# Kernel tuning notes

Measured on AMD Instinct MI355X. Metric: run time of the kernel, lower is better.

## Reference

```python
import jax, jax.numpy as jnp
import numpy as np

BATCH, G, E, D = 8192, 3, 32, 128  # batch, genres-per-sample, num experts, feature dim


def setup_inputs() -> dict:
    key = jax.random.key(0)
    k1, k2, k3, k4 = jax.random.split(key, 4)
    x = jax.random.normal(k1, (BATCH, D), dtype=jnp.float32)
    genres = jax.random.randint(k2, (BATCH, G), 0, E, dtype=jnp.int64)
    W0 = jax.random.normal(k3, (E, D, D), dtype=jnp.float32)
    W1 = jax.random.normal(k4, (E, D, D), dtype=jnp.float32)
    return {"x": x, "genres": genres, "W0": W0, "W1": W1}


def _moe_layer(x, genres, W):
    # gather per-token expert weights: [B, G, in, out]
    ew = W[genres]
    # mask: genre index 0 means padding slot
    mask = (genres != 0)[..., None].astype(x.dtype)  # [B, G, 1]
    # 'bij,bijk->bik' with x broadcast over the genre axis
    y = jnp.einsum('bi,bgio->bgo', x, ew) * mask      # [B, G, out]
    cnt = jnp.clip(jnp.sum(mask, axis=1), 1e-9)       # [B, 1]
    return jax.nn.leaky_relu(jnp.sum(y, axis=1) / cnt, negative_slope=0.01)


def reference(x, genres, W0, W1):
    x = _moe_layer(x, genres, W0)
    x = _moe_layer(x, genres, W1)
    return x
```

## Files before the change

kernel.cpp:

```cpp
#include <hip/hip_runtime.h>

#define BATCH 8192
#define NG 3
#define NE 32
#define D 128
#define NPAIR (BATCH * NG)
#define TILE 32
#define CHUNK 2048
#define NCHUNK (NPAIR / CHUNK)
#define NFIN (BATCH * 16 / 256)

typedef __attribute__((ext_vector_type(8))) short short8;
typedef __attribute__((ext_vector_type(4))) float f32x4;

#define OFF_YB   0
#define OFF_YB2  ((size_t)NPAIR * D * 2)
#define WS_REQUIRED (OFF_YB2 + (size_t)NPAIR * D * 2)

static __device__ __forceinline__ ushort f2bf(float f) {
    unsigned b = __float_as_uint(f);
    unsigned r = (b + 0x7FFFu + ((b >> 16) & 1u)) >> 16;
    return (ushort)r;
}
static __device__ __forceinline__ float bf2f(ushort u) {
    return __uint_as_float(((unsigned)u) << 16);
}
static __device__ __forceinline__ unsigned pk2(float lo, float hi) {
    return (unsigned)f2bf(lo) | ((unsigned)f2bf(hi) << 16);
}

template<int LAYER>
static __device__ __forceinline__ void gemm_body(
    const float* __restrict__ x, const ushort* __restrict__ ybin,
    const int* __restrict__ genres, const float* __restrict__ W,
    ushort* __restrict__ ydst)
{
    const int e = blockIdx.y + 1;
    const int pbase = blockIdx.x * CHUNK;

    __shared__ ushort sW[D * D];
    __shared__ ushort sX[TILE * D];
    __shared__ int list[CHUNK];
    __shared__ int scnt;

    const int tid = threadIdx.x;
    if (tid == 0) scnt = 0;
    __syncthreads();

    #pragma unroll
    for (int i = 0; i < CHUNK / 256; ++i) {
        int p = pbase + i * 256 + tid;
        if (genres[p] == e) {
            int idx = atomicAdd(&scnt, 1);
            list[idx] = p;
        }
    }

    const float* Ws = W + (size_t)e * D * D;
    char* sWb = (char*)sW;
    #pragma unroll
    for (int i = 0; i < 16; ++i) {
        int idx = i * 256 + tid;
        int c = idx & 127;
        int k4 = idx >> 7;
        float a0 = Ws[(size_t)(4 * k4 + 0) * D + c];
        float a1 = Ws[(size_t)(4 * k4 + 1) * D + c];
        float a2 = Ws[(size_t)(4 * k4 + 2) * D + c];
        float a3 = Ws[(size_t)(4 * k4 + 3) * D + c];
        int byteoff = (c * 256 + k4 * 8) ^ ((c & 7) << 4);
        uint2 q = { pk2(a0, a1), pk2(a2, a3) };
        *(uint2*)(sWb + byteoff) = q;
    }
    __syncthreads();

    const int ntotal = scnt;
    const int wave = tid >> 6, lane = tid & 63;
    const int g = lane >> 4, l15 = lane & 15;
    char* sXb = (char*)sX;

    for (int t0 = 0; t0 < ntotal; t0 += TILE) {
        const int nt = min(TILE, ntotal - t0);
        __syncthreads();

        {
            const int t = tid >> 3, th = tid & 7;
            int p = list[t0 + ((t < nt) ? t : 0)];
            int row = p / NG;
            int g0 = genres[row * NG + 0];
            int g1 = genres[row * NG + 1];
            int g2 = genres[row * NG + 2];
            int cnt = (g0 != 0) + (g1 != 0) + (g2 != 0);
            float scale = 1.0f / (float)((cnt > 0) ? cnt : 1);
            unsigned q[8];
            if (LAYER == 1) {
                const float* xp = x + (size_t)row * D + th * 16;
                float v[16];
                *(float4*)&v[0]  = *(const float4*)(xp);
                *(float4*)&v[4]  = *(const float4*)(xp + 4);
                *(float4*)&v[8]  = *(const float4*)(xp + 8);
                *(float4*)&v[12] = *(const float4*)(xp + 12);
                #pragma unroll
                for (int j = 0; j < 8; ++j)
                    q[j] = pk2(v[2*j] * scale, v[2*j+1] * scale);
            } else {
                float s[16];
                #pragma unroll
                for (int j = 0; j < 16; ++j) s[j] = 0.0f;
                #pragma unroll
                for (int slot = 0; slot < NG; ++slot) {
                    int gg = (slot == 0) ? g0 : (slot == 1) ? g1 : g2;
                    if (gg != 0) {
                        const ushort* yp = ybin + ((size_t)row * NG + slot) * D + th * 16;
                        uint4 va = *(const uint4*)yp;
                        uint4 vb = *(const uint4*)(yp + 8);
                        unsigned w[8] = { va.x, va.y, va.z, va.w,
                                          vb.x, vb.y, vb.z, vb.w };
                        #pragma unroll
                        for (int j = 0; j < 8; ++j) {
                            s[2*j]   += bf2f((ushort)(w[j] & 0xFFFF));
                            s[2*j+1] += bf2f((ushort)(w[j] >> 16));
                        }
                    }
                }
                #pragma unroll
                for (int j = 0; j < 8; ++j) {
                    float lo = s[2*j],  hi = s[2*j+1];
                    lo = ((lo >= 0.f) ? lo : 0.01f * lo) * scale;
                    hi = ((hi >= 0.f) ? hi : 0.01f * hi) * scale;
                    q[j] = pk2(lo, hi);
                }
            }
            int b0 = (t * 256 + (th * 2) * 16)     ^ ((t & 7) << 4);
            int b1 = (t * 256 + (th * 2 + 1) * 16) ^ ((t & 7) << 4);
            *(uint4*)(sXb + b0) = make_uint4(q[0], q[1], q[2], q[3]);
            *(uint4*)(sXb + b1) = make_uint4(q[4], q[5], q[6], q[7]);
        }
        __syncthreads();

        f32x4 acc00 = {0.f,0.f,0.f,0.f}, acc01 = {0.f,0.f,0.f,0.f};
        f32x4 acc10 = {0.f,0.f,0.f,0.f}, acc11 = {0.f,0.f,0.f,0.f};

        #pragma unroll
        for (int ks = 0; ks < 4; ++ks) {
            const int kb = ks * 64 + g * 16;
            int c0 = wave * 32 + l15, c1 = c0 + 16;
            short8 a0 = *(const short8*)(sWb + ((c0 * 256 + kb) ^ ((c0 & 7) << 4)));
            short8 a1 = *(const short8*)(sWb + ((c1 * 256 + kb) ^ ((c1 & 7) << 4)));
            int t0l = l15, t1l = l15 + 16;
            short8 b0 = *(const short8*)(sXb + ((t0l * 256 + kb) ^ ((t0l & 7) << 4)));
            short8 b1 = *(const short8*)(sXb + ((t1l * 256 + kb) ^ ((t1l & 7) << 4)));
            acc00 = __builtin_amdgcn_mfma_f32_16x16x32_bf16(a0, b0, acc00, 0, 0, 0);
            acc01 = __builtin_amdgcn_mfma_f32_16x16x32_bf16(a0, b1, acc01, 0, 0, 0);
            acc10 = __builtin_amdgcn_mfma_f32_16x16x32_bf16(a1, b0, acc10, 0, 0, 0);
            acc11 = __builtin_amdgcn_mfma_f32_16x16x32_bf16(a1, b1, acc11, 0, 0, 0);
        }

        #pragma unroll
        for (int n = 0; n < 2; ++n) {
            int tok = n * 16 + l15;
            if (tok < nt) {
                int p = list[t0 + tok];
                ushort* dst = ydst + (size_t)p * D + wave * 32 + g * 4;
                f32x4 v0 = (n == 0) ? acc00 : acc01;
                f32x4 v1 = (n == 0) ? acc10 : acc11;
                ushort4 p0 = { f2bf(v0[0]), f2bf(v0[1]), f2bf(v0[2]), f2bf(v0[3]) };
                ushort4 p1 = { f2bf(v1[0]), f2bf(v1[1]), f2bf(v1[2]), f2bf(v1[3]) };
                *(ushort4*)(dst)      = p0;
                *(ushort4*)(dst + 16) = p1;
            }
        }
    }
}

__global__ __launch_bounds__(256, 3) void moe_gemm1_kernel(
    const float* __restrict__ x, const int* __restrict__ genres,
    const float* __restrict__ W0, ushort* __restrict__ yb)
{
    gemm_body<1>(x, nullptr, genres, W0, yb);
}

__global__ __launch_bounds__(256, 3) void moe_gemm2_kernel(
    const ushort* __restrict__ yb, const int* __restrict__ genres,
    const float* __restrict__ W1, ushort* __restrict__ yb2)
{
    gemm_body<2>(nullptr, yb, genres, W1, yb2);
}

__global__ __launch_bounds__(256) void moe_final_kernel(
    const ushort* __restrict__ yb2, const int* __restrict__ genres,
    float* __restrict__ out)
{
    int gid = blockIdx.x * 256 + threadIdx.x;
    int b = gid >> 4, c8 = (gid & 15) * 8;
    int g0 = genres[b * NG + 0];
    int g1 = genres[b * NG + 1];
    int g2 = genres[b * NG + 2];

    float s[8] = {0,0,0,0,0,0,0,0};
    #pragma unroll
    for (int slot = 0; slot < NG; ++slot) {
        int g = (slot == 0) ? g0 : (slot == 1) ? g1 : g2;
        if (g != 0) {
            uint4 v = *(const uint4*)&yb2[((size_t)b * NG + slot) * D + c8];
            const unsigned w[4] = { v.x, v.y, v.z, v.w };
            #pragma unroll
            for (int j = 0; j < 4; ++j) {
                s[2*j]   += bf2f((ushort)(w[j] & 0xFFFF));
                s[2*j+1] += bf2f((ushort)(w[j] >> 16));
            }
        }
    }
    float r[8];
    #pragma unroll
    for (int j = 0; j < 8; ++j)
        r[j] = (s[j] >= 0.f) ? s[j] : 0.01f * s[j];
    float4 lo = { r[0], r[1], r[2], r[3] };
    float4 hi = { r[4], r[5], r[6], r[7] };
    *(float4*)&out[(size_t)b * D + c8]     = lo;
    *(float4*)&out[(size_t)b * D + c8 + 4] = hi;
}

__global__ __launch_bounds__(128) void moe_layer_kernel(
    const float* __restrict__ x, const int* __restrict__ genres,
    const float* __restrict__ W, float* __restrict__ out)
{
    const int b = blockIdx.x;
    const int o = threadIdx.x;
    __shared__ float xs[D];
    xs[o] = x[(size_t)b * D + o];
    __syncthreads();
    int e0 = genres[b * NG + 0], e1 = genres[b * NG + 1], e2 = genres[b * NG + 2];
    float acc = 0.0f; int cnt = 0;
    #pragma unroll
    for (int g = 0; g < NG; ++g) {
        int e = (g == 0) ? e0 : (g == 1) ? e1 : e2;
        if (e != 0) {
            ++cnt;
            const float* We = W + (size_t)e * D * D + o;
            float a = 0.0f;
            #pragma unroll 8
            for (int i = 0; i < D; ++i) a = fmaf(xs[i], We[(size_t)i * D], a);
            acc += a;
        }
    }
    float r = (cnt > 0) ? (acc / (float)cnt) : 0.0f;
    out[(size_t)b * D + o] = (r >= 0.0f) ? r : 0.01f * r;
}

extern "C" void kernel_launch(void* const* d_in, const int* in_sizes, int n_in,
                              void* d_out, int out_size, void* d_ws, size_t ws_size,
                              hipStream_t stream)
{
    const float* x      = (const float*)d_in[0];
    const int*   genres = (const int*)d_in[1];
    const float* W0     = (const float*)d_in[2];
    const float* W1     = (const float*)d_in[3];
    float*       out    = (float*)d_out;

    if (ws_size < WS_REQUIRED) {
        moe_layer_kernel<<<BATCH, D, 0, stream>>>(x,   genres, W0, out);
        moe_layer_kernel<<<BATCH, D, 0, stream>>>(out, genres, W1, out);
        return;
    }

    char* ws = (char*)d_ws;
    ushort* yb  = (ushort*)(ws + OFF_YB);
    ushort* yb2 = (ushort*)(ws + OFF_YB2);

    dim3 ggrid(NCHUNK, NE - 1);
    moe_gemm1_kernel<<<ggrid, 256, 0, stream>>>(x, genres, W0, yb);
    moe_gemm2_kernel<<<ggrid, 256, 0, stream>>>(yb, genres, W1, yb2);
    moe_final_kernel<<<NFIN, 256, 0, stream>>>(yb2, genres, out);
}
```

Measured before the change: 33.48 us.

## Split expert GEMM output columns across two blocks and vectorize genre scan

Each chunk/expert block now computes only half of the output columns, so the grid doubles and per-block shared weight storage halves, allowing higher occupancy (launch bounds raised to 4). The genre scan reads int4 vectors, and blocks with no matching tokens exit before loading weights. The cost is that the activation tile (gather, scale, leaky_relu for layer 2) is recomputed by both column halves, and each wave now issues fewer MFMAs per tile.

```diff
diff --git a/kernel.cpp b/kernel.cpp
--- a/kernel.cpp
+++ b/kernel.cpp
@@ -35,10 +35,12 @@
     const int* __restrict__ genres, const float* __restrict__ W,
     ushort* __restrict__ ydst)
 {
+    const int bx = blockIdx.x;
+    const int chunk = bx >> 1, hcol = bx & 1;
     const int e = blockIdx.y + 1;
-    const int pbase = blockIdx.x * CHUNK;
-
-    __shared__ ushort sW[D * D];
+    const int pbase = chunk * CHUNK;
+
+    __shared__ ushort sW[64 * D];
     __shared__ ushort sX[TILE * D];
     __shared__ int list[CHUNK];
     __shared__ int scnt;
@@ -47,22 +49,27 @@
     if (tid == 0) scnt = 0;
     __syncthreads();
 
-    #pragma unroll
-    for (int i = 0; i < CHUNK / 256; ++i) {
-        int p = pbase + i * 256 + tid;
-        if (genres[p] == e) {
-            int idx = atomicAdd(&scnt, 1);
-            list[idx] = p;
-        }
-    }
-
-    const float* Ws = W + (size_t)e * D * D;
+    const int4* g4 = (const int4*)(genres + pbase);
+    #pragma unroll
+    for (int i = 0; i < CHUNK / 1024; ++i) {
+        int4 gv = g4[i * 256 + tid];
+        int p = pbase + (i * 256 + tid) * 4;
+        if (gv.x == e) list[atomicAdd(&scnt, 1)] = p + 0;
+        if (gv.y == e) list[atomicAdd(&scnt, 1)] = p + 1;
+        if (gv.z == e) list[atomicAdd(&scnt, 1)] = p + 2;
+        if (gv.w == e) list[atomicAdd(&scnt, 1)] = p + 3;
+    }
+    __syncthreads();
+    const int ntotal = scnt;
+    if (ntotal == 0) return;
+
+    const float* Ws = W + (size_t)e * D * D + hcol * 64;
     char* sWb = (char*)sW;
     #pragma unroll
-    for (int i = 0; i < 16; ++i) {
+    for (int i = 0; i < 8; ++i) {
         int idx = i * 256 + tid;
-        int c = idx & 127;
-        int k4 = idx >> 7;
+        int c = idx & 63;
+        int k4 = idx >> 6;
         float a0 = Ws[(size_t)(4 * k4 + 0) * D + c];
         float a1 = Ws[(size_t)(4 * k4 + 1) * D + c];
         float a2 = Ws[(size_t)(4 * k4 + 2) * D + c];
@@ -71,11 +78,10 @@
         uint2 q = { pk2(a0, a1), pk2(a2, a3) };
         *(uint2*)(sWb + byteoff) = q;
     }
-    __syncthreads();
-
-    const int ntotal = scnt;
+
     const int wave = tid >> 6, lane = tid & 63;
     const int g = lane >> 4, l15 = lane & 15;
+    const int colb = wave * 16;
     char* sXb = (char*)sX;
 
     for (int t0 = 0; t0 < ntotal; t0 += TILE) {
@@ -137,22 +143,18 @@
         }
         __syncthreads();
 
-        f32x4 acc00 = {0.f,0.f,0.f,0.f}, acc01 = {0.f,0.f,0.f,0.f};
-        f32x4 acc10 = {0.f,0.f,0.f,0.f}, acc11 = {0.f,0.f,0.f,0.f};
+        f32x4 acc0 = {0.f,0.f,0.f,0.f}, acc1 = {0.f,0.f,0.f,0.f};
 
         #pragma unroll
         for (int ks = 0; ks < 4; ++ks) {
             const int kb = ks * 64 + g * 16;
-            int c0 = wave * 32 + l15, c1 = c0 + 16;
+            int c0 = colb + l15;
             short8 a0 = *(const short8*)(sWb + ((c0 * 256 + kb) ^ ((c0 & 7) << 4)));
-            short8 a1 = *(const short8*)(sWb + ((c1 * 256 + kb) ^ ((c1 & 7) << 4)));
             int t0l = l15, t1l = l15 + 16;
             short8 b0 = *(const short8*)(sXb + ((t0l * 256 + kb) ^ ((t0l & 7) << 4)));
             short8 b1 = *(const short8*)(sXb + ((t1l * 256 + kb) ^ ((t1l & 7) << 4)));
-            acc00 = __builtin_amdgcn_mfma_f32_16x16x32_bf16(a0, b0, acc00, 0, 0, 0);
-            acc01 = __builtin_amdgcn_mfma_f32_16x16x32_bf16(a0, b1, acc01, 0, 0, 0);
-            acc10 = __builtin_amdgcn_mfma_f32_16x16x32_bf16(a1, b0, acc10, 0, 0, 0);
-            acc11 = __builtin_amdgcn_mfma_f32_16x16x32_bf16(a1, b1, acc11, 0, 0, 0);
+            acc0 = __builtin_amdgcn_mfma_f32_16x16x32_bf16(a0, b0, acc0, 0, 0, 0);
+            acc1 = __builtin_amdgcn_mfma_f32_16x16x32_bf16(a0, b1, acc1, 0, 0, 0);
         }
 
         #pragma unroll
@@ -160,26 +162,23 @@
             int tok = n * 16 + l15;
             if (tok < nt) {
                 int p = list[t0 + tok];
-                ushort* dst = ydst + (size_t)p * D + wave * 32 + g * 4;
-                f32x4 v0 = (n == 0) ? acc00 : acc01;
-                f32x4 v1 = (n == 0) ? acc10 : acc11;
-                ushort4 p0 = { f2bf(v0[0]), f2bf(v0[1]), f2bf(v0[2]), f2bf(v0[3]) };
-                ushort4 p1 = { f2bf(v1[0]), f2bf(v1[1]), f2bf(v1[2]), f2bf(v1[3]) };
-                *(ushort4*)(dst)      = p0;
-                *(ushort4*)(dst + 16) = p1;
+                ushort* dst = ydst + (size_t)p * D + hcol * 64 + colb + g * 4;
+                f32x4 v = (n == 0) ? acc0 : acc1;
+                ushort4 pq = { f2bf(v[0]), f2bf(v[1]), f2bf(v[2]), f2bf(v[3]) };
+                *(ushort4*)dst = pq;
             }
         }
     }
 }
 
-__global__ __launch_bounds__(256, 3) void moe_gemm1_kernel(
+__global__ __launch_bounds__(256, 4) void moe_gemm1_kernel(
     const float* __restrict__ x, const int* __restrict__ genres,
     const float* __restrict__ W0, ushort* __restrict__ yb)
 {
     gemm_body<1>(x, nullptr, genres, W0, yb);
 }
 
-__global__ __launch_bounds__(256, 3) void moe_gemm2_kernel(
+__global__ __launch_bounds__(256, 4) void moe_gemm2_kernel(
     const ushort* __restrict__ yb, const int* __restrict__ genres,
     const float* __restrict__ W1, ushort* __restrict__ yb2)
 {
@@ -267,7 +266,7 @@
     ushort* yb  = (ushort*)(ws + OFF_YB);
     ushort* yb2 = (ushort*)(ws + OFF_YB2);
 
-    dim3 ggrid(NCHUNK, NE - 1);
+    dim3 ggrid(NCHUNK * 2, NE - 1);
     moe_gemm1_kernel<<<ggrid, 256, 0, stream>>>(x, genres, W0, yb);
     moe_gemm2_kernel<<<ggrid, 256, 0, stream>>>(yb, genres, W1, yb2);
     moe_final_kernel<<<NFIN, 256, 0, stream>>>(yb2, genres, out);
```

Result: faster. 31.19 us (-6.8%).
